# Kernel optimization log

Hardware: AMD Instinct MI355X
Metric: run time of the kernel (lower is better)

## Reference

```python
import jax, jax.numpy as jnp
import numpy as np

TEMPERATURE = 0.05
EPS = 1e-6
N, D = 8192, 64


def setup_inputs() -> dict:
    key = jax.random.key(0)
    k1, k2 = jax.random.split(key)
    anchor_embeddings = jax.random.normal(k1, (N, D), dtype=jnp.float32)
    positive_embeddings = jax.random.normal(k2, (N, D), dtype=jnp.float32)
    return {"anchor_embeddings": anchor_embeddings,
            "positive_embeddings": positive_embeddings}


def _cos_matrix(x, y, nx, ny):
    # pairwise cosine sim with torch CosineSimilarity eps semantics:
    # dot / max(||x||*||y||, eps)
    return (x @ y.T) / jnp.maximum(nx[:, None] * ny[None, :], EPS)


def reference(anchor_embeddings, positive_embeddings):
    a, p = anchor_embeddings, positive_embeddings
    na = jnp.linalg.norm(a, axis=-1)  # [N]
    npn = jnp.linalg.norm(p, axis=-1)  # [N]

    inv_t = 1.0 / TEMPERATURE
    S_ap = _cos_matrix(a, p, na, npn)  # [N, N]
    S_aa = _cos_matrix(a, a, na, na)   # [N, N]
    S_pp = _cos_matrix(p, p, npn, npn)  # [N, N]

    E_ap = jnp.exp(S_ap * inv_t)
    E_aa = jnp.exp(S_aa * inv_t)
    E_pp = jnp.exp(S_pp * inv_t)

    self_term = jnp.exp(jnp.asarray(inv_t, dtype=a.dtype))  # exp(1/T)
    # partition_i = sum_j E_ap[i,j] + sum_j E_aa[i,j] - e^{1/T}
    #             + sum_j E_ap[j,i] + sum_j E_pp[j,i] - e^{1/T}
    partition = (E_ap.sum(axis=1) + E_aa.sum(axis=1)
                 + E_ap.sum(axis=0) + E_pp.sum(axis=0)
                 - 2.0 * self_term)

    # loss = -mean_i log( exp(cos(a_i,p_i)/T) / partition_i )
    pos_logit = jnp.diagonal(S_ap) * inv_t
    loss = -jnp.mean(pos_logit - jnp.log(partition))
    return loss
```

## Files before the change

### kernel.cpp

```cpp
#include <hip/hip_runtime.h>
#include <hip/hip_bf16.h>
#include <math.h>

#define N 8192
#define D 64
#define INVT 20.0f
#define EPS 1e-6f
#define ZSCALE 5.3715835f

typedef __attribute__((ext_vector_type(8))) short bf16x8;
typedef __attribute__((ext_vector_type(4))) float f32x4;

#if __has_builtin(__builtin_amdgcn_exp2f)
#define EXP2F(x) __builtin_amdgcn_exp2f(x)
#else
#define EXP2F(x) exp2f(x)
#endif


__device__ __forceinline__ void unrank(int t, int& bi, int& bj) {
    int b = (int)((257.0f - sqrtf(66049.0f - 8.0f * (float)t)) * 0.5f);
    while (b * (257 - b) / 2 > t) --b;
    while ((b + 1) * (256 - b) / 2 <= t) ++b;
    bi = b;
    bj = b + (t - b * (257 - b) / 2);
}

__global__ __launch_bounds__(256) void prep_kernel(
    const float* __restrict__ A, const float* __restrict__ P,
    __hip_bfloat16* __restrict__ Zn, float* __restrict__ diag20,
    float* __restrict__ part, float* __restrict__ lacc, unsigned* __restrict__ cnt) {
    if (blockIdx.x < 64) part[blockIdx.x * 256 + threadIdx.x] = 0.0f;
    else if (blockIdx.x == 64 && threadIdx.x == 0) { *lacc = 0.0f; *cnt = 0u; }

    const int lane = threadIdx.x & 63;
    const int w    = threadIdx.x >> 6;
    const int r    = blockIdx.x * 4 + w;
    const int u    = lane >> 3, sub = lane & 7;
    const int upos = (u >> 2) * 64 + (u & 3) * 16;

    float a = A[r * D + lane];
    float p = P[r * D + lane];
    float sa = a * a, sp = p * p, dp = a * p;
    #pragma unroll
    for (int off = 1; off < 64; off <<= 1) {
        sa += __shfl_xor(sa, off, 64);
        sp += __shfl_xor(sp, off, 64);
        dp += __shfl_xor(dp, off, 64);
    }
    float na  = sqrtf(sa);
    float npn = sqrtf(sp);
    {
        int g = r >> 4, l2 = r & 15;
        Zn[(g * 128 + upos + l2) * 8 + sub] = __float2bfloat16(a * (ZSCALE / na));
    }
    {
        int R = N + r; int g = R >> 4, l2 = R & 15;
        Zn[(g * 128 + upos + l2) * 8 + sub] = __float2bfloat16(p * (ZSCALE / npn));
    }
    if (lane == 0)
        diag20[r] = (dp / fmaxf(na * npn, EPS)) * INVT;
}

__global__ __launch_bounds__(256, 4) void tiles_kernel(
    const __hip_bfloat16* __restrict__ Zn, float* __restrict__ part) {
    __shared__ float rs[4][16][68];
    __shared__ float merged[2][128];
    __shared__ float cmerged[2][2][64];

    const int tid = threadIdx.x;
    const int lane = tid & 63, w = tid >> 6;
    const int wr = w >> 1, wc = w & 1;
    const int ln = lane & 15, q = lane >> 4;
    const bf16x8* Zf = (const bf16x8*)Zn;

    const int b = (int)blockIdx.x;
    const int wgid = (b & 7) * 516 + (b >> 3);
    const int t0 = 2 * wgid;
    const int t1 = t0 + 1;
    int bi0, bj0, bi1, bj1;
    unrank(t0, bi0, bj0);
    unrank(t1, bi1, bj1);

    const f32x4 zero = {0.0f, 0.0f, 0.0f, 0.0f};

    bf16x8 af0[4][2], bv0[4][2];
    #pragma unroll
    for (int ii = 0; ii < 4; ++ii) {
        int ga = bi0 * 8 + wr * 4 + ii;
        int gb = bj0 * 8 + wc * 4 + ii;
        #pragma unroll
        for (int kc = 0; kc < 2; ++kc) {
            af0[ii][kc] = Zf[ga * 128 + kc * 64 + lane];
            bv0[ii][kc] = Zf[gb * 128 + kc * 64 + lane];
        }
    }

    const bool dwave0 = (bi0 == bj0) && (wr == wc);
    float csum[4] = {0.0f, 0.0f, 0.0f, 0.0f};
    #pragma unroll
    for (int ii = 0; ii < 4; ++ii) {
        f32x4 acc[4];
        #pragma unroll
        for (int jj = 0; jj < 4; ++jj)
            acc[jj] = __builtin_amdgcn_mfma_f32_16x16x32_bf16(
                af0[ii][0], bv0[jj][0], zero, 0, 0, 0);
        #pragma unroll
        for (int jj = 0; jj < 4; ++jj)
            acc[jj] = __builtin_amdgcn_mfma_f32_16x16x32_bf16(
                af0[ii][1], bv0[jj][1], acc[jj], 0, 0, 0);

        f32x4 rsum_ii = {};
        #pragma unroll
        for (int jj = 0; jj < 4; ++jj) {
            f32x4 e;
            #pragma unroll
            for (int r = 0; r < 4; ++r) e[r] = EXP2F(acc[jj][r]);
            if (dwave0 && (ii == jj)) {
                #pragma unroll
                for (int r = 0; r < 4; ++r)
                    if (ln == q * 4 + r) e[r] = 0.0f;
            }
            rsum_ii += e;
            csum[jj] += (e[0] + e[1]) + (e[2] + e[3]);
        }
        *(f32x4*)&rs[w][ln][ii * 16 + q * 4] = rsum_ii;
    }

    bf16x8 af1[4][2], bv1[4][2];
    #pragma unroll
    for (int ii = 0; ii < 4; ++ii) {
        int gb = bj1 * 8 + wc * 4 + ii;
        #pragma unroll
        for (int kc = 0; kc < 2; ++kc)
            bv1[ii][kc] = Zf[gb * 128 + kc * 64 + lane];
    }
    if (bi1 == bi0) {
        #pragma unroll
        for (int ii = 0; ii < 4; ++ii) {
            af1[ii][0] = af0[ii][0];
            af1[ii][1] = af0[ii][1];
        }
    } else {
        #pragma unroll
        for (int ii = 0; ii < 4; ++ii) {
            int ga = bi1 * 8 + wr * 4 + ii;
            #pragma unroll
            for (int kc = 0; kc < 2; ++kc)
                af1[ii][kc] = Zf[ga * 128 + kc * 64 + lane];
        }
    }

    {
        float rowsum = 0.0f;
        #pragma unroll
        for (int l = 0; l < 16; ++l) rowsum += rs[w][l][lane];
        merged[wc][wr * 64 + lane] = rowsum;

        float cs0 = csum[0], cs1 = csum[1], cs2 = csum[2], cs3 = csum[3];
        cs0 += __shfl_xor(cs0, 16, 64); cs0 += __shfl_xor(cs0, 32, 64);
        cs1 += __shfl_xor(cs1, 16, 64); cs1 += __shfl_xor(cs1, 32, 64);
        cs2 += __shfl_xor(cs2, 16, 64); cs2 += __shfl_xor(cs2, 32, 64);
        cs3 += __shfl_xor(cs3, 16, 64); cs3 += __shfl_xor(cs3, 32, 64);
        float cval = (q == 0) ? cs0 : (q == 1) ? cs1 : (q == 2) ? cs2 : cs3;
        cmerged[wr][wc][q * 16 + ln] = cval;
        __syncthreads();

        if (tid < 128) {
            atomicAdd(part + bi0 * 128 + tid, merged[0][tid] + merged[1][tid]);
        } else if (bi0 != bj0) {
            int col = tid - 128;
            atomicAdd(part + bj0 * 128 + col,
                      cmerged[0][col >> 6][col & 63] + cmerged[1][col >> 6][col & 63]);
        }
    }

    const bool dwave1 = (bi1 == bj1) && (wr == wc);
    float csumB[4] = {0.0f, 0.0f, 0.0f, 0.0f};
    #pragma unroll
    for (int ii = 0; ii < 4; ++ii) {
        f32x4 acc[4];
        #pragma unroll
        for (int jj = 0; jj < 4; ++jj)
            acc[jj] = __builtin_amdgcn_mfma_f32_16x16x32_bf16(
                af1[ii][0], bv1[jj][0], zero, 0, 0, 0);
        #pragma unroll
        for (int jj = 0; jj < 4; ++jj)
            acc[jj] = __builtin_amdgcn_mfma_f32_16x16x32_bf16(
                af1[ii][1], bv1[jj][1], acc[jj], 0, 0, 0);

        f32x4 rsum_ii = {};
        #pragma unroll
        for (int jj = 0; jj < 4; ++jj) {
            f32x4 e;
            #pragma unroll
            for (int r = 0; r < 4; ++r) e[r] = EXP2F(acc[jj][r]);
            if (dwave1 && (ii == jj)) {
                #pragma unroll
                for (int r = 0; r < 4; ++r)
                    if (ln == q * 4 + r) e[r] = 0.0f;
            }
            rsum_ii += e;
            csumB[jj] += (e[0] + e[1]) + (e[2] + e[3]);
        }
        *(f32x4*)&rs[w][ln][ii * 16 + q * 4] = rsum_ii;
    }

    __syncthreads();

    {
        float rowsum = 0.0f;
        #pragma unroll
        for (int l = 0; l < 16; ++l) rowsum += rs[w][l][lane];
        merged[wc][wr * 64 + lane] = rowsum;

        float cs0 = csumB[0], cs1 = csumB[1], cs2 = csumB[2], cs3 = csumB[3];
        cs0 += __shfl_xor(cs0, 16, 64); cs0 += __shfl_xor(cs0, 32, 64);
        cs1 += __shfl_xor(cs1, 16, 64); cs1 += __shfl_xor(cs1, 32, 64);
        cs2 += __shfl_xor(cs2, 16, 64); cs2 += __shfl_xor(cs2, 32, 64);
        cs3 += __shfl_xor(cs3, 16, 64); cs3 += __shfl_xor(cs3, 32, 64);
        float cval = (q == 0) ? cs0 : (q == 1) ? cs1 : (q == 2) ? cs2 : cs3;
        cmerged[wr][wc][q * 16 + ln] = cval;
        __syncthreads();

        if (tid < 128) {
            atomicAdd(part + bi1 * 128 + tid, merged[0][tid] + merged[1][tid]);
        } else if (bi1 != bj1) {
            int col = tid - 128;
            atomicAdd(part + bj1 * 128 + col,
                      cmerged[0][col >> 6][col & 63] + cmerged[1][col >> 6][col & 63]);
        }
    }
}

__global__ __launch_bounds__(256) void loss_kernel(
    const float* __restrict__ part, const float* __restrict__ diag20,
    float* __restrict__ lacc, unsigned* __restrict__ cnt, float* __restrict__ out) {
    int i = blockIdx.x * 256 + threadIdx.x;
    float v = logf(part[i] + part[N + i]) - diag20[i];
    #pragma unroll
    for (int off = 32; off > 0; off >>= 1) v += __shfl_down(v, off, 64);
    __shared__ float wsm[4];
    int lane = threadIdx.x & 63, wv = threadIdx.x >> 6;
    if (lane == 0) wsm[wv] = v;
    __syncthreads();
    if (threadIdx.x == 0) {
        atomicAdd(lacc, wsm[0] + wsm[1] + wsm[2] + wsm[3]);
        __threadfence();
        unsigned old = atomicAdd(cnt, 1u);
        if (old == (N / 256 - 1)) {
            float tot = atomicAdd(lacc, 0.0f);
            out[0] = tot * (1.0f / (float)N);
        }
    }
}

extern "C" void kernel_launch(void* const* d_in, const int* in_sizes, int n_in,
                              void* d_out, int out_size, void* d_ws, size_t ws_size,
                              hipStream_t stream) {
    const float* A = (const float*)d_in[0];
    const float* P = (const float*)d_in[1];

    __hip_bfloat16* Zn = (__hip_bfloat16*)d_ws;
    float* diag20 = (float*)((char*)d_ws + 2u * N * D * sizeof(__hip_bfloat16));
    float* part   = diag20 + N;
    float* lacc   = part + 2 * N;
    unsigned* cnt = (unsigned*)(lacc + 1);

    prep_kernel<<<N / 4, 256, 0, stream>>>(A, P, Zn, diag20, part, lacc, cnt);

    const int nblocks = 128 * 129 / 4;
    tiles_kernel<<<nblocks, 256, 0, stream>>>(Zn, part);

    loss_kernel<<<N / 256, 256, 0, stream>>>(part, diag20, lacc, cnt, (float*)d_out);
}
```

Baseline: 98.16 us.

## Privatize partition accumulators per XCD and drop block-to-XCD remapping

Each workgroup reads its hardware XCC ID and atomically accumulates row and column partition sums into a private copy of the partition array for that XCD, rather than one shared global array. The loss kernel then sums the eight copies. The aim is to cut cross-die atomic contention and coherence traffic. The earlier blockIdx remap that grouped tiles by XCD is removed, so adjacent tiles now run round-robin across XCDs, which may reduce L2 reuse of Zn tiles. It also adds more zeroing work and extra reads in the loss kernel.

```diff
diff --git a/kernel.cpp b/kernel.cpp
--- a/kernel.cpp
+++ b/kernel.cpp
@@ -7,6 +7,7 @@
 #define INVT 20.0f
 #define EPS 1e-6f
 #define ZSCALE 5.3715835f
+#define NXCD 8
 
 typedef __attribute__((ext_vector_type(8))) short bf16x8;
 typedef __attribute__((ext_vector_type(4))) float f32x4;
@@ -29,9 +30,9 @@
 __global__ __launch_bounds__(256) void prep_kernel(
     const float* __restrict__ A, const float* __restrict__ P,
     __hip_bfloat16* __restrict__ Zn, float* __restrict__ diag20,
-    float* __restrict__ part, float* __restrict__ lacc, unsigned* __restrict__ cnt) {
-    if (blockIdx.x < 64) part[blockIdx.x * 256 + threadIdx.x] = 0.0f;
-    else if (blockIdx.x == 64 && threadIdx.x == 0) { *lacc = 0.0f; *cnt = 0u; }
+    float* __restrict__ part8, float* __restrict__ lacc, unsigned* __restrict__ cnt) {
+    if (blockIdx.x < 512) part8[blockIdx.x * 256 + threadIdx.x] = 0.0f;
+    else if (blockIdx.x == 512 && threadIdx.x == 0) { *lacc = 0.0f; *cnt = 0u; }
 
     const int lane = threadIdx.x & 63;
     const int w    = threadIdx.x >> 6;
@@ -63,7 +64,7 @@
 }
 
 __global__ __launch_bounds__(256, 4) void tiles_kernel(
-    const __hip_bfloat16* __restrict__ Zn, float* __restrict__ part) {
+    const __hip_bfloat16* __restrict__ Zn, float* __restrict__ part8) {
     __shared__ float rs[4][16][68];
     __shared__ float merged[2][128];
     __shared__ float cmerged[2][2][64];
@@ -74,9 +75,11 @@
     const int ln = lane & 15, q = lane >> 4;
     const bf16x8* Zf = (const bf16x8*)Zn;
 
-    const int b = (int)blockIdx.x;
-    const int wgid = (b & 7) * 516 + (b >> 3);
-    const int t0 = 2 * wgid;
+    unsigned xcc;
+    asm volatile("s_getreg_b32 %0, hwreg(HW_REG_XCC_ID)" : "=s"(xcc));
+    float* __restrict__ myp = part8 + (size_t)(xcc & (NXCD - 1)) * (2 * N);
+
+    const int t0 = 2 * (int)blockIdx.x;
     const int t1 = t0 + 1;
     int bi0, bj0, bi1, bj1;
     unrank(t0, bi0, bj0);
@@ -167,10 +170,10 @@
         __syncthreads();
 
         if (tid < 128) {
-            atomicAdd(part + bi0 * 128 + tid, merged[0][tid] + merged[1][tid]);
+            atomicAdd(myp + bi0 * 128 + tid, merged[0][tid] + merged[1][tid]);
         } else if (bi0 != bj0) {
             int col = tid - 128;
-            atomicAdd(part + bj0 * 128 + col,
+            atomicAdd(myp + bj0 * 128 + col,
                       cmerged[0][col >> 6][col & 63] + cmerged[1][col >> 6][col & 63]);
         }
     }
@@ -224,20 +227,24 @@
         __syncthreads();
 
         if (tid < 128) {
-            atomicAdd(part + bi1 * 128 + tid, merged[0][tid] + merged[1][tid]);
+            atomicAdd(myp + bi1 * 128 + tid, merged[0][tid] + merged[1][tid]);
         } else if (bi1 != bj1) {
             int col = tid - 128;
-            atomicAdd(part + bj1 * 128 + col,
+            atomicAdd(myp + bj1 * 128 + col,
                       cmerged[0][col >> 6][col & 63] + cmerged[1][col >> 6][col & 63]);
         }
     }
 }
 
 __global__ __launch_bounds__(256) void loss_kernel(
-    const float* __restrict__ part, const float* __restrict__ diag20,
+    const float* __restrict__ part8, const float* __restrict__ diag20,
     float* __restrict__ lacc, unsigned* __restrict__ cnt, float* __restrict__ out) {
     int i = blockIdx.x * 256 + threadIdx.x;
-    float v = logf(part[i] + part[N + i]) - diag20[i];
+    float s = 0.0f;
+    #pragma unroll
+    for (int x = 0; x < NXCD; ++x)
+        s += part8[x * 2 * N + i] + part8[x * 2 * N + N + i];
+    float v = logf(s) - diag20[i];
     #pragma unroll
     for (int off = 32; off > 0; off >>= 1) v += __shfl_down(v, off, 64);
     __shared__ float wsm[4];
@@ -263,14 +270,15 @@
 
     __hip_bfloat16* Zn = (__hip_bfloat16*)d_ws;
     float* diag20 = (float*)((char*)d_ws + 2u * N * D * sizeof(__hip_bfloat16));
-    float* part   = diag20 + N;
-    float* lacc   = part + 2 * N;
+    float* part8  = diag20 + N;
+    float* lacc   = part8 + NXCD * 2 * N;
     unsigned* cnt = (unsigned*)(lacc + 1);
 
-    prep_kernel<<<N / 4, 256, 0, stream>>>(A, P, Zn, diag20, part, lacc, cnt);
+    prep_kernel<<<N / 4, 256, 0, stream>>>(A, P, Zn, diag20, part8, lacc, cnt);
 
     const int nblocks = 128 * 129 / 4;
-    tiles_kernel<<<nblocks, 256, 0, stream>>>(Zn, part);
-
-    loss_kernel<<<N / 256, 256, 0, stream>>>(part, diag20, lacc, cnt, (float*)d_out);
-}
+    tiles_kernel<<<nblocks, 256, 0, stream>>>(Zn, part8);
+
+    loss_kernel<<<N / 256, 256, 0, stream>>>(part8, diag20, lacc, cnt,
+                                             (float*)d_out);
+}
```

Measured after the change: 97.81 us. No clear change (-0.4%).
